# Performance work log

Measured on AMD Instinct MI355X. Metric: run time of the kernel, lower is better.

Reference implementation:

```python
import jax, jax.numpy as jnp
import numpy as np

NUM_GRAPHS = 8
NEG_SLOPE = 0.2


def add_self_loops(edge_index, n):
    loops = jnp.arange(n, dtype=edge_index.dtype)
    src = jnp.concatenate([edge_index[0], loops])
    dst = jnp.concatenate([edge_index[1], loops])
    return src, dst


def gat_conv(x, src, dst, W, att_src, att_dst, bias, concat):
    # x: [N, F_in]; W: [F_in, H*C]; att_src/att_dst: [H, C]; bias: [H*C] or [C]
    n = x.shape[0]
    H, C = att_src.shape
    xl = (x @ W).reshape(n, H, C)                     # [N, H, C]
    a_src = jnp.einsum('nhc,hc->nh', xl, att_src)     # [N, H]
    a_dst = jnp.einsum('nhc,hc->nh', xl, att_dst)     # [N, H]
    e = jax.nn.leaky_relu(a_src[src] + a_dst[dst], NEG_SLOPE)  # [E, H]
    # segment softmax over edges grouped by destination node
    m = jax.ops.segment_max(e, dst, num_segments=n)   # [N, H]
    e = jnp.exp(e - m[dst])
    denom = jax.ops.segment_sum(e, dst, num_segments=n)
    alpha = e / (denom[dst] + 1e-16)                  # [E, H]
    msg = xl[src] * alpha[:, :, None]                 # [E, H, C]
    out = jax.ops.segment_sum(msg, dst, num_segments=n)  # [N, H, C]
    out = out.reshape(n, H * C) if concat else out.mean(axis=1)
    return out + bias


def global_mean_pool(x, batch, num_graphs):
    s = jax.ops.segment_sum(x, batch, num_segments=num_graphs)
    cnt = jax.ops.segment_sum(jnp.ones((x.shape[0],), x.dtype), batch, num_segments=num_graphs)
    return s / jnp.maximum(cnt, 1.0)[:, None]


def setup_inputs() -> dict:
    key = jax.random.key(0)
    ks = jax.random.split(key, 12)
    N, E, F_in, Ch, H, F_out = 50000, 800000, 128, 64, 4, 128
    x = jax.random.normal(ks[0], (N, F_in), dtype=jnp.float32)
    edge_index = jax.random.randint(ks[1], (2, E), 0, N, dtype=jnp.int64)
    batch = jnp.sort(jax.random.randint(ks[2], (N,), 0, NUM_GRAPHS, dtype=jnp.int64))
    s = 0.1
    W1 = jax.random.normal(ks[3], (F_in, H * Ch), dtype=jnp.float32) * s
    att_src1 = jax.random.normal(ks[4], (H, Ch), dtype=jnp.float32) * s
    att_dst1 = jax.random.normal(ks[5], (H, Ch), dtype=jnp.float32) * s
    bias1 = jnp.zeros((H * Ch,), dtype=jnp.float32)
    W2 = jax.random.normal(ks[6], (H * Ch, F_out), dtype=jnp.float32) * s
    att_src2 = jax.random.normal(ks[7], (1, F_out), dtype=jnp.float32) * s
    att_dst2 = jax.random.normal(ks[8], (1, F_out), dtype=jnp.float32) * s
    bias2 = jnp.zeros((F_out,), dtype=jnp.float32)
    return {"x": x, "edge_index": edge_index, "batch": batch,
            "W1": W1, "att_src1": att_src1, "att_dst1": att_dst1, "bias1": bias1,
            "W2": W2, "att_src2": att_src2, "att_dst2": att_dst2, "bias2": bias2}


def reference(x, edge_index, batch, W1, att_src1, att_dst1, bias1, W2, att_src2, att_dst2, bias2):
    n = x.shape[0]
    src, dst = add_self_loops(edge_index, n)
    h = gat_conv(x, src, dst, W1, att_src1, att_dst1, bias1, concat=True)
    h = jax.nn.relu(h)
    h = gat_conv(h, src, dst, W2, att_src2, att_dst2, bias2, concat=False)
    return global_mean_pool(h, batch, NUM_GRAPHS)
```

## Files before the change

kernel.cpp:

```cpp
#include <hip/hip_runtime.h>
#include <cstdint>
#include <cstddef>

#define NEG_SLOPE 0.2f
#define LOG2E 1.44269504088896f

typedef __attribute__((ext_vector_type(8))) short bf16x8;
typedef __attribute__((ext_vector_type(4))) float f32x4;
typedef __attribute__((ext_vector_type(2))) float f32x2;

__device__ __forceinline__ ushort f2b(float f) {
  unsigned u = __float_as_uint(f);
  return (ushort)((u + 0x7FFFu + ((u >> 16) & 1)) >> 16);
}
__device__ __forceinline__ float fexp2(float x) {
#if __has_builtin(__builtin_amdgcn_exp2f)
  return __builtin_amdgcn_exp2f(x);
#else
  return __exp2f(x);
#endif
}
__device__ __forceinline__ int lbound(const int* __restrict__ a, int n, int key) {
  int lo = 0, hi = n;
  while (lo < hi) { int m = (lo + hi) >> 1; if (a[m] < key) lo = m + 1; else hi = m; }
  return lo;
}

__global__ __launch_bounds__(256) void pack_w_both(const float* __restrict__ W1,
                                                   ushort* __restrict__ Bp1,
                                                   const float* __restrict__ W2,
                                                   ushort* __restrict__ Bp2) {
  int i = blockIdx.x * 256 + threadIdx.x;
  if (i >= 128 * 256) return;
  {
    int k = i >> 8, n = i & 255;
    Bp1[(((size_t)(k >> 3) * 256 + n) << 3) + (k & 7)] = f2b(W1[i]);
  }
  {
    int k = i >> 7, n = i & 127;
    Bp2[(((size_t)(k >> 3) * 128 + n) << 3) + (k & 7)] = f2b(W2[i]);
  }
}

template<int N, int K, int C, int H, bool AF32>
__global__ __launch_bounds__(256) void gemm_attn(const void* __restrict__ A_,
                                                 const ushort* __restrict__ Bp,
                                                 const float* __restrict__ att_src,
                                                 const float* __restrict__ att_dst,
                                                 unsigned char* __restrict__ C8,
                                                 float* __restrict__ a_src,
                                                 float* __restrict__ a_dst, int M) {
  const int wave = threadIdx.x >> 6;
  const int lane = threadIdx.x & 63;
  const int strips = M / 16;
  const int strip = blockIdx.x * 4 + wave;
  if (strip >= strips) return;
  const int r = lane & 15, kg = lane >> 4;
  const int row = strip * 16 + r;

  bf16x8 a[K / 32];
  if constexpr (AF32) {
    const float* Af = (const float*)A_;
    #pragma unroll
    for (int k0 = 0; k0 < K / 32; ++k0) {
      float4 f0 = *(const float4*)(Af + (size_t)row * K + k0 * 32 + kg * 8);
      float4 f1 = *(const float4*)(Af + (size_t)row * K + k0 * 32 + kg * 8 + 4);
      bf16x8 t;
      t[0] = (short)f2b(f0.x); t[1] = (short)f2b(f0.y);
      t[2] = (short)f2b(f0.z); t[3] = (short)f2b(f0.w);
      t[4] = (short)f2b(f1.x); t[5] = (short)f2b(f1.y);
      t[6] = (short)f2b(f1.z); t[7] = (short)f2b(f1.w);
      a[k0] = t;
    }
  } else {
    const ushort* Ab = (const ushort*)A_;
    #pragma unroll
    for (int k0 = 0; k0 < K / 32; ++k0)
      a[k0] = *(const bf16x8*)(Ab + (size_t)row * K + k0 * 32 + kg * 8);
  }

  float as_part[4] = {}, ad_part[4] = {};
  #pragma unroll 2
  for (int n0 = 0; n0 < N / 16; ++n0) {
    f32x4 acc = {0.f, 0.f, 0.f, 0.f};
    #pragma unroll
    for (int k0 = 0; k0 < K / 32; ++k0) {
      bf16x8 b = *(const bf16x8*)(Bp + ((size_t)(k0 * 4 + kg) * N + n0 * 16 + r) * 8);
      acc = __builtin_amdgcn_mfma_f32_16x16x32_bf16(a[k0], b, acc, 0, 0, 0);
    }
    float asv = att_src[n0 * 16 + r] * LOG2E;
    float adv = att_dst[n0 * 16 + r] * LOG2E;
    #pragma unroll
    for (int i = 0; i < 4; ++i) {
      as_part[i] = fmaf(acc[i], asv, as_part[i]);
      ad_part[i] = fmaf(acc[i], adv, ad_part[i]);
    }
    #pragma unroll
    for (int i = 0; i < 4; ++i) {
      int pk = __builtin_amdgcn_cvt_pk_fp8_f32(acc[i], acc[i], 0, false);
      C8[((size_t)strip * 16 + kg * 4 + i) * N + n0 * 16 + r] = (unsigned char)(pk & 0xFF);
    }
    if (((n0 + 1) * 16) % C == 0) {
      int h = (n0 * 16) / C;
      #pragma unroll
      for (int i = 0; i < 4; ++i) {
        float ts = as_part[i], td = ad_part[i];
        #pragma unroll
        for (int off = 1; off < 16; off <<= 1) {
          ts += __shfl_xor(ts, off);
          td += __shfl_xor(td, off);
        }
        if (r == i) {
          a_src[(size_t)(strip * 16 + kg * 4 + i) * H + h] = ts;
          a_dst[(size_t)(strip * 16 + kg * 4 + i) * H + h] = td;
        }
        as_part[i] = 0.f;
        ad_part[i] = 0.f;
      }
    }
  }
}

__global__ __launch_bounds__(256) void rank_k(const int* __restrict__ edst,
                                              int* __restrict__ hist,
                                              int* __restrict__ rank, int E) {
  int e = blockIdx.x * 256 + threadIdx.x;
  if (e >= E) return;
  rank[e] = atomicAdd(hist + edst[e], 1);
}

__global__ __launch_bounds__(256) void scan1_k(const int* __restrict__ hist,
                                               int* __restrict__ excl,
                                               int* __restrict__ chunksum, int n) {
  __shared__ int sums[256];
  int base = blockIdx.x * 1024 + threadIdx.x * 4;
  int4 v = {0, 0, 0, 0};
  if (base + 3 < n) v = *(const int4*)(hist + base);
  else {
    if (base < n)     v.x = hist[base];
    if (base + 1 < n) v.y = hist[base + 1];
    if (base + 2 < n) v.z = hist[base + 2];
    if (base + 3 < n) v.w = hist[base + 3];
  }
  int s = v.x + v.y + v.z + v.w;
  sums[threadIdx.x] = s;
  __syncthreads();
  for (int off = 1; off < 256; off <<= 1) {
    int t = (threadIdx.x >= (unsigned)off) ? sums[threadIdx.x - off] : 0;
    __syncthreads();
    sums[threadIdx.x] += t;
    __syncthreads();
  }
  if (threadIdx.x == 255) chunksum[blockIdx.x] = sums[255];
  int e0 = sums[threadIdx.x] - s;
  int e1 = e0 + v.x, e2 = e1 + v.y, e3 = e2 + v.z;
  if (base + 3 < n) {
    int4 o = {e0, e1, e2, e3};
    *(int4*)(excl + base) = o;
  } else {
    if (base < n)     excl[base] = e0;
    if (base + 1 < n) excl[base + 1] = e1;
    if (base + 2 < n) excl[base + 2] = e2;
    if (base + 3 < n) excl[base + 3] = e3;
  }
}

__global__ void scan2_k(const int* __restrict__ chunksum,
                        int* __restrict__ chunkoff, int nchunks) {
  if (threadIdx.x == 0) {
    int run = 0;
    for (int c = 0; c < nchunks; ++c) { chunkoff[c] = run; run += chunksum[c]; }
  }
}

__global__ __launch_bounds__(256) void addoff_k(int* __restrict__ rowptr,
                                                const int* __restrict__ chunkoff,
                                                int n, int total) {
  int i = blockIdx.x * 256 + threadIdx.x;
  if (i == 0) rowptr[n] = total;
  if (i >= n) return;
  rowptr[i] += chunkoff[i >> 10];
}

__global__ __launch_bounds__(256) void fill_k(const int* __restrict__ esrc,
                                              const int* __restrict__ edst,
                                              const int* __restrict__ rowptr,
                                              const int* __restrict__ rank,
                                              int* __restrict__ csr_src,
                                              int E, int Epad) {
  int e = blockIdx.x * 256 + threadIdx.x;
  if (e < E) csr_src[rowptr[edst[e]] + rank[e]] = esrc[e];
  else if (e < Epad) csr_src[e] = 0;
}

template<int H, int C>
__global__ __launch_bounds__(256) void agg1_k(const int* __restrict__ rowptr,
                                              const int* __restrict__ csr,
                                              const float* __restrict__ a_src,
                                              const float* __restrict__ a_dst,
                                              const unsigned char* __restrict__ xl,
                                              const float* __restrict__ bias,
                                              ushort* __restrict__ out, int n) {
  constexpr int F = H * C;
  const int wid0 = (blockIdx.x * 256 + threadIdx.x) >> 6;
  if (wid0 >= n) return;
  const int wid = __builtin_amdgcn_readfirstlane(wid0);
  const int lane = threadIdx.x & 63;
  const int h = lane >> 4;
  const uint lofs = (uint)lane * 4;
  const int j4 = lane & 3;
  const int je = lane >> 2;
  const int beg = rowptr[wid];
  const int end = rowptr[wid + 1];

  const float adh_s = a_dst[(uint)wid * 4 + j4];
  float vs_s = a_src[(uint)wid * 4 + j4] + adh_s;
  vs_s = fmaxf(vs_s, NEG_SLOPE * vs_s);

  float den = 1.f;
  float acc[4];
  {
    uint xs = *(const uint*)(xl + ((uint)wid * F + lofs));
    f32x2 lo = __builtin_amdgcn_cvt_pk_f32_fp8(xs, false);
    f32x2 hi = __builtin_amdgcn_cvt_pk_f32_fp8(xs, true);
    acc[0] = lo[0]; acc[1] = lo[1]; acc[2] = hi[0]; acc[3] = hi[1];
  }

  for (int j = beg; j < end; j += 16) {
    int sl = csr[j + je];
    float t = a_src[(uint)sl * 4 + j4] + adh_s;
    t = fmaxf(t, NEG_SLOPE * t);
    t = (j + je < end) ? t - vs_s : -1e30f;
    float pl = fexp2(t);
    uint xv[16];
    #pragma unroll
    for (int u = 0; u < 16; ++u) {
      int su = csr[j + u];
      xv[u] = *(const uint*)(xl + ((uint)su * F + lofs));
    }
    #pragma unroll
    for (int u = 0; u < 16; ++u) {
      float pu = __shfl(pl, u * 4 + h);
      den += pu;
      f32x2 lo = __builtin_amdgcn_cvt_pk_f32_fp8(xv[u], false);
      f32x2 hi = __builtin_amdgcn_cvt_pk_f32_fp8(xv[u], true);
      acc[0] = fmaf(pu, lo[0], acc[0]);
      acc[1] = fmaf(pu, lo[1], acc[1]);
      acc[2] = fmaf(pu, hi[0], acc[2]);
      acc[3] = fmaf(pu, hi[1], acc[3]);
    }
  }

  float inv = 1.f / (den + 1e-16f);
  float o[4];
  #pragma unroll
  for (int i = 0; i < 4; ++i)
    o[i] = fmaxf(fmaf(acc[i], inv, bias[lane * 4 + i]), 0.f);
  ushort4 ov = {f2b(o[0]), f2b(o[1]), f2b(o[2]), f2b(o[3])};
  *(ushort4*)(out + (size_t)wid * F + lane * 4) = ov;
}

__global__ __launch_bounds__(256) void agg2_k(const int* __restrict__ rowptr,
                                              const int* __restrict__ csr,
                                              const float* __restrict__ a_src,
                                              const float* __restrict__ a_dst,
                                              const unsigned char* __restrict__ xl,
                                              float* __restrict__ out2,
                                              int n, int Emax) {
  const int pair = (blockIdx.x * 256 + threadIdx.x) >> 6;
  const int lane = threadIdx.x & 63;
  const int l32 = lane & 31;
  const int half = lane >> 5;
  int wid = pair * 2 + half;
  const bool act = wid < n;
  if (!act) wid = n - 1;
  const uint lofs = (uint)l32 * 4;
  const int beg = rowptr[wid];
  const int deg = rowptr[wid + 1] - beg;
  const int mdeg = max(deg, __shfl_xor(deg, 32));
  const float adh = a_dst[wid];

  float vs = a_src[wid] + adh;
  vs = fmaxf(vs, NEG_SLOPE * vs);
  float den = 1.f;
  float acc[4];
  {
    uint xs = *(const uint*)(xl + ((uint)wid * 128 + lofs));
    f32x2 lo = __builtin_amdgcn_cvt_pk_f32_fp8(xs, false);
    f32x2 hi = __builtin_amdgcn_cvt_pk_f32_fp8(xs, true);
    acc[0] = lo[0]; acc[1] = lo[1]; acc[2] = hi[0]; acc[3] = hi[1];
  }

  for (int j = 0; j < mdeg; j += 32) {
    int sl = csr[min(beg + j + l32, Emax)];
    float t = a_src[sl] + adh;
    t = fmaxf(t, NEG_SLOPE * t);
    t = (j + l32 < deg) ? t - vs : -1e30f;
    float pl = fexp2(t);
    #pragma unroll
    for (int g = 0; g < 2; ++g) {
      int su[16];
      uint xv[16];
      #pragma unroll
      for (int u = 0; u < 16; ++u) {
        su[u] = __shfl(sl, half * 32 + g * 16 + u);
        xv[u] = *(const uint*)(xl + ((uint)su[u] * 128 + lofs));
      }
      #pragma unroll
      for (int u = 0; u < 16; ++u) {
        float pu = __shfl(pl, half * 32 + g * 16 + u);
        den += pu;
        f32x2 lo = __builtin_amdgcn_cvt_pk_f32_fp8(xv[u], false);
        f32x2 hi = __builtin_amdgcn_cvt_pk_f32_fp8(xv[u], true);
        acc[0] = fmaf(pu, lo[0], acc[0]);
        acc[1] = fmaf(pu, lo[1], acc[1]);
        acc[2] = fmaf(pu, hi[0], acc[2]);
        acc[3] = fmaf(pu, hi[1], acc[3]);
      }
    }
  }

  if (act) {
    float inv = 1.f / (den + 1e-16f);
    float4 ov = {acc[0] * inv, acc[1] * inv, acc[2] * inv, acc[3] * inv};
    *(float4*)(out2 + (size_t)wid * 128 + l32 * 4) = ov;
  }
}

__global__ __launch_bounds__(256) void pool2_k(const float* __restrict__ out2,
                                               const int* __restrict__ batch,
                                               float* __restrict__ pp, int n) {
  const int g = blockIdx.y;
  const int b = blockIdx.x;
  const int lo = lbound(batch, n, g);
  const int hi = lbound(batch, n, g + 1);
  const int cnt = hi - lo;
  const int span = (cnt + 31) >> 5;
  const int s0 = lo + b * span;
  const int s1 = min(s0 + span, hi);
  const int qid = threadIdx.x & 31;
  const int phase = threadIdx.x >> 5;

  float4 a = {0.f, 0.f, 0.f, 0.f};
  for (int node = s0 + phase; node < s1; node += 8) {
    float4 v = *(const float4*)(out2 + (size_t)node * 128 + qid * 4);
    a.x += v.x; a.y += v.y; a.z += v.z; a.w += v.w;
  }
  __shared__ float red[8][128];
  *(float4*)&red[phase][qid * 4] = a;
  __syncthreads();
  if (threadIdx.x < 128) {
    float s = 0.f;
    #pragma unroll
    for (int ph = 0; ph < 8; ++ph) s += red[ph][threadIdx.x];
    pp[((size_t)g * 32 + b) * 128 + threadIdx.x] = s;
  }
}

__global__ __launch_bounds__(256) void finalize_k(const float* __restrict__ pp,
                                                  const int* __restrict__ batch,
                                                  const float* __restrict__ bias2,
                                                  float* __restrict__ out, int n) {
  int t = blockIdx.x * 256 + threadIdx.x;
  if (t >= 8 * 128) return;
  int g = t >> 7, c = t & 127;
  float s = 0.f;
  #pragma unroll
  for (int b = 0; b < 32; ++b) s += pp[((size_t)g * 32 + b) * 128 + c];
  int lo = lbound(batch, n, g);
  int hi = lbound(batch, n, g + 1);
  float cnt = (float)(hi - lo);
  out[t] = s / fmaxf(cnt, 1.f) + bias2[c];
}

extern "C" void kernel_launch(void* const* d_in, const int* in_sizes, int n_in,
                              void* d_out, int out_size, void* d_ws, size_t ws_size,
                              hipStream_t stream) {
  const float* x        = (const float*)d_in[0];
  const int*   ei       = (const int*)d_in[1];
  const int*   batch    = (const int*)d_in[2];
  const float* W1       = (const float*)d_in[3];
  const float* att_src1 = (const float*)d_in[4];
  const float* att_dst1 = (const float*)d_in[5];
  const float* bias1    = (const float*)d_in[6];
  const float* W2       = (const float*)d_in[7];
  const float* att_src2 = (const float*)d_in[8];
  const float* att_dst2 = (const float*)d_in[9];
  const float* bias2    = (const float*)d_in[10];
  float* out = (float*)d_out;

  const int E  = in_sizes[1] / 2;
  const int NN = in_sizes[2];
  const int* esrc = ei;
  const int* edst = ei + E;
  const int PAD = 64;

  char* w = (char*)d_ws;
  size_t woff = 0;
  auto walloc = [&](size_t bytes) -> char* {
    char* r = w + woff;
    woff += (bytes + 255) & ~(size_t)255;
    return r;
  };
  unsigned char* xl1 = (unsigned char*)walloc((size_t)NN * 256);
  ushort* h1     = (ushort*)walloc((size_t)NN * 256 * 2);
  unsigned char* xl2 = (unsigned char*)walloc((size_t)NN * 128);
  float*  a_src1 = (float*)walloc((size_t)NN * 4 * 4);
  float*  a_dst1 = (float*)walloc((size_t)NN * 4 * 4);
  float*  a_src2 = (float*)walloc((size_t)NN * 4);
  float*  a_dst2 = (float*)walloc((size_t)NN * 4);
  int*    rowptr = (int*)walloc((size_t)(NN + 1) * 4);
  int*    hist   = (int*)walloc((size_t)NN * 4);
  int*    rank   = (int*)walloc((size_t)E * 4);
  int*    csrsrc = (int*)walloc((size_t)(E + PAD) * 4);
  ushort* Bp1    = (ushort*)walloc(128 * 256 * 2);
  ushort* Bp2    = (ushort*)walloc(256 * 128 * 2);
  int*    chunks = (int*)walloc(256 * 4);
  int*    chunko = (int*)walloc(256 * 4);
  float*  pp     = (float*)walloc(8 * 32 * 128 * 4);
  float*  out2   = (float*)h1;

  dim3 blk(256);
  const int nbE  = (E + 255) / 256;
  const int nbEp = (E + PAD + 255) / 256;
  const int nbN4 = (NN + 3) / 4;
  const int nbP  = ((NN + 1) / 2 + 3) / 4;
  const int nchunks = (NN + 1023) / 1024;
  const int gblocks = (NN / 16 + 3) / 4;

  hipMemsetAsync(hist, 0, (size_t)NN * 4, stream);
  rank_k<<<nbE, blk, 0, stream>>>(edst, hist, rank, E);
  scan1_k<<<nchunks, blk, 0, stream>>>(hist, rowptr, chunks, NN);
  scan2_k<<<1, 64, 0, stream>>>(chunks, chunko, nchunks);
  addoff_k<<<(NN + 255) / 256, blk, 0, stream>>>(rowptr, chunko, NN, E);
  fill_k<<<nbEp, blk, 0, stream>>>(esrc, edst, rowptr, rank, csrsrc, E, E + PAD);

  pack_w_both<<<(128 * 256 + 255) / 256, blk, 0, stream>>>(W1, Bp1, W2, Bp2);

  gemm_attn<256, 128, 64, 4, true><<<gblocks, blk, 0, stream>>>(
      x, Bp1, att_src1, att_dst1, xl1, a_src1, a_dst1, NN);
  agg1_k<4, 64><<<nbN4, blk, 0, stream>>>(
      rowptr, csrsrc, a_src1, a_dst1, xl1, bias1, h1, NN);

  gemm_attn<128, 256, 128, 1, false><<<gblocks, blk, 0, stream>>>(
      h1, Bp2, att_src2, att_dst2, xl2, a_src2, a_dst2, NN);
  agg2_k<<<nbP, blk, 0, stream>>>(
      rowptr, csrsrc, a_src2, a_dst2, xl2, out2, NN, E + PAD - 1);

  {
    dim3 grid2(32, 8);
    pool2_k<<<grid2, blk, 0, stream>>>(out2, batch, pp, NN);
  }
  finalize_k<<<4, blk, 0, stream>>>(pp, batch, bias2, out, NN);
}
```

Before: 188.9 us.

## Fuse setup kernels, rank into GEMM launch, single-block scan, pooling into agg2

Merges the weight packing, histogram memset and pool-buffer zeroing into one setup kernel. The edge-rank atomics now run as extra blocks of the first GEMM launch, and the three-kernel scan becomes a single 1024-thread block. The second aggregation reduces its outputs per graph in shared memory and atomically adds them into 64 replicated partial buffers, which removes the out2 write/read and the separate pool kernel. This cuts launch count and memory traffic, at the cost of a serial single-block scan and of atomic contention in the pool.

```diff
diff --git a/kernel.cpp b/kernel.cpp
--- a/kernel.cpp
+++ b/kernel.cpp
@@ -4,6 +4,7 @@
 
 #define NEG_SLOPE 0.2f
 #define LOG2E 1.44269504088896f
+#define NREP 64
 
 typedef __attribute__((ext_vector_type(8))) short bf16x8;
 typedef __attribute__((ext_vector_type(4))) float f32x4;
@@ -26,34 +27,41 @@
   return lo;
 }
 
-__global__ __launch_bounds__(256) void pack_w_both(const float* __restrict__ W1,
-                                                   ushort* __restrict__ Bp1,
-                                                   const float* __restrict__ W2,
-                                                   ushort* __restrict__ Bp2) {
+__global__ __launch_bounds__(256) void setup_k(const float* __restrict__ W1,
+                                               ushort* __restrict__ Bp1,
+                                               const float* __restrict__ W2,
+                                               ushort* __restrict__ Bp2,
+                                               int* __restrict__ hist,
+                                               float* __restrict__ pp, int n) {
   int i = blockIdx.x * 256 + threadIdx.x;
-  if (i >= 128 * 256) return;
   {
-    int k = i >> 8, n = i & 255;
-    Bp1[(((size_t)(k >> 3) * 256 + n) << 3) + (k & 7)] = f2b(W1[i]);
+    int k = i >> 8, c = i & 255;
+    Bp1[(((size_t)(k >> 3) * 256 + c) << 3) + (k & 7)] = f2b(W1[i]);
   }
   {
-    int k = i >> 7, n = i & 127;
-    Bp2[(((size_t)(k >> 3) * 128 + n) << 3) + (k & 7)] = f2b(W2[i]);
-  }
+    int k = i >> 7, c = i & 127;
+    Bp2[(((size_t)(k >> 3) * 128 + c) << 3) + (k & 7)] = f2b(W2[i]);
+  }
+  if (i < n) hist[i] = 0;
+  int i2 = i + 32768;
+  if (i2 < n) hist[i2] = 0;
+  pp[i] = 0.f;
+  pp[i + 32768] = 0.f;
 }
 
 template<int N, int K, int C, int H, bool AF32>
-__global__ __launch_bounds__(256) void gemm_attn(const void* __restrict__ A_,
-                                                 const ushort* __restrict__ Bp,
-                                                 const float* __restrict__ att_src,
-                                                 const float* __restrict__ att_dst,
-                                                 unsigned char* __restrict__ C8,
-                                                 float* __restrict__ a_src,
-                                                 float* __restrict__ a_dst, int M) {
+__device__ __forceinline__ void gemm_attn_body(const void* __restrict__ A_,
+                                               const ushort* __restrict__ Bp,
+                                               const float* __restrict__ att_src,
+                                               const float* __restrict__ att_dst,
+                                               unsigned char* __restrict__ C8,
+                                               float* __restrict__ a_src,
+                                               float* __restrict__ a_dst,
+                                               int M, int bid) {
   const int wave = threadIdx.x >> 6;
   const int lane = threadIdx.x & 63;
   const int strips = M / 16;
-  const int strip = blockIdx.x * 4 + wave;
+  const int strip = bid * 4 + wave;
   if (strip >= strips) return;
   const int r = lane & 15, kg = lane >> 4;
   const int row = strip * 16 + r;
@@ -121,65 +129,64 @@
   }
 }
 
-__global__ __launch_bounds__(256) void rank_k(const int* __restrict__ edst,
-                                              int* __restrict__ hist,
-                                              int* __restrict__ rank, int E) {
-  int e = blockIdx.x * 256 + threadIdx.x;
-  if (e >= E) return;
-  rank[e] = atomicAdd(hist + edst[e], 1);
-}
-
-__global__ __launch_bounds__(256) void scan1_k(const int* __restrict__ hist,
-                                               int* __restrict__ excl,
-                                               int* __restrict__ chunksum, int n) {
-  __shared__ int sums[256];
-  int base = blockIdx.x * 1024 + threadIdx.x * 4;
-  int4 v = {0, 0, 0, 0};
-  if (base + 3 < n) v = *(const int4*)(hist + base);
-  else {
-    if (base < n)     v.x = hist[base];
-    if (base + 1 < n) v.y = hist[base + 1];
-    if (base + 2 < n) v.z = hist[base + 2];
-    if (base + 3 < n) v.w = hist[base + 3];
-  }
-  int s = v.x + v.y + v.z + v.w;
-  sums[threadIdx.x] = s;
+template<int N, int K, int C, int H, bool AF32>
+__global__ __launch_bounds__(256) void gemm_rank_k(const void* __restrict__ A_,
+                                                   const ushort* __restrict__ Bp,
+                                                   const float* __restrict__ att_src,
+                                                   const float* __restrict__ att_dst,
+                                                   unsigned char* __restrict__ C8,
+                                                   float* __restrict__ a_src,
+                                                   float* __restrict__ a_dst, int M,
+                                                   const int* __restrict__ edst,
+                                                   int* __restrict__ hist,
+                                                   int* __restrict__ rank,
+                                                   int E, int GB) {
+  if ((int)blockIdx.x < GB) {
+    gemm_attn_body<N, K, C, H, AF32>(A_, Bp, att_src, att_dst, C8, a_src, a_dst,
+                                     M, blockIdx.x);
+  } else {
+    int base = ((blockIdx.x - GB) * 256 + threadIdx.x) * 8;
+    #pragma unroll
+    for (int u = 0; u < 8; ++u) {
+      int e = base + u;
+      if (e < E) rank[e] = atomicAdd(hist + edst[e], 1);
+    }
+  }
+}
+
+template<int N, int K, int C, int H, bool AF32>
+__global__ __launch_bounds__(256) void gemm_attn_k(const void* __restrict__ A_,
+                                                   const ushort* __restrict__ Bp,
+                                                   const float* __restrict__ att_src,
+                                                   const float* __restrict__ att_dst,
+                                                   unsigned char* __restrict__ C8,
+                                                   float* __restrict__ a_src,
+                                                   float* __restrict__ a_dst, int M) {
+  gemm_attn_body<N, K, C, H, AF32>(A_, Bp, att_src, att_dst, C8, a_src, a_dst,
+                                   M, blockIdx.x);
+}
+
+__global__ __launch_bounds__(1024) void scan_fused_k(const int* __restrict__ hist,
+                                                     int* __restrict__ rowptr,
+                                                     int n, int total) {
+  __shared__ int sums[1024];
+  const int t = threadIdx.x;
+  const int per = (n + 1023) / 1024;
+  const int s0 = min(t * per, n);
+  const int s1 = min(s0 + per, n);
+  int s = 0;
+  for (int i = s0; i < s1; ++i) s += hist[i];
+  sums[t] = s;
   __syncthreads();
-  for (int off = 1; off < 256; off <<= 1) {
-    int t = (threadIdx.x >= (unsigned)off) ? sums[threadIdx.x - off] : 0;
+  for (int off = 1; off < 1024; off <<= 1) {
+    int v = (t >= off) ? sums[t - off] : 0;
     __syncthreads();
-    sums[threadIdx.x] += t;
+    sums[t] += v;
     __syncthreads();
   }
-  if (threadIdx.x == 255) chunksum[blockIdx.x] = sums[255];
-  int e0 = sums[threadIdx.x] - s;
-  int e1 = e0 + v.x, e2 = e1 + v.y, e3 = e2 + v.z;
-  if (base + 3 < n) {
-    int4 o = {e0, e1, e2, e3};
-    *(int4*)(excl + base) = o;
-  } else {
-    if (base < n)     excl[base] = e0;
-    if (base + 1 < n) excl[base + 1] = e1;
-    if (base + 2 < n) excl[base + 2] = e2;
-    if (base + 3 < n) excl[base + 3] = e3;
-  }
-}
-
-__global__ void scan2_k(const int* __restrict__ chunksum,
-                        int* __restrict__ chunkoff, int nchunks) {
-  if (threadIdx.x == 0) {
-    int run = 0;
-    for (int c = 0; c < nchunks; ++c) { chunkoff[c] = run; run += chunksum[c]; }
-  }
-}
-
-__global__ __launch_bounds__(256) void addoff_k(int* __restrict__ rowptr,
-                                                const int* __restrict__ chunkoff,
-                                                int n, int total) {
-  int i = blockIdx.x * 256 + threadIdx.x;
-  if (i == 0) rowptr[n] = total;
-  if (i >= n) return;
-  rowptr[i] += chunkoff[i >> 10];
+  int run = sums[t] - s;
+  for (int i = s0; i < s1; ++i) { rowptr[i] = run; run += hist[i]; }
+  if (t == 0) rowptr[n] = total;
 }
 
 __global__ __launch_bounds__(256) void fill_k(const int* __restrict__ esrc,
@@ -260,13 +267,14 @@
   *(ushort4*)(out + (size_t)wid * F + lane * 4) = ov;
 }
 
-__global__ __launch_bounds__(256) void agg2_k(const int* __restrict__ rowptr,
-                                              const int* __restrict__ csr,
-                                              const float* __restrict__ a_src,
-                                              const float* __restrict__ a_dst,
-                                              const unsigned char* __restrict__ xl,
-                                              float* __restrict__ out2,
-                                              int n, int Emax) {
+__global__ __launch_bounds__(256) void agg2pool_k(const int* __restrict__ rowptr,
+                                                  const int* __restrict__ csr,
+                                                  const float* __restrict__ a_src,
+                                                  const float* __restrict__ a_dst,
+                                                  const unsigned char* __restrict__ xl,
+                                                  const int* __restrict__ batch,
+                                                  float* __restrict__ pp,
+                                                  int n, int Emax) {
   const int pair = (blockIdx.x * 256 + threadIdx.x) >> 6;
   const int lane = threadIdx.x & 63;
   const int l32 = lane & 31;
@@ -320,40 +328,30 @@
     }
   }
 
-  if (act) {
-    float inv = 1.f / (den + 1e-16f);
-    float4 ov = {acc[0] * inv, acc[1] * inv, acc[2] * inv, acc[3] * inv};
-    *(float4*)(out2 + (size_t)wid * 128 + l32 * 4) = ov;
-  }
-}
-
-__global__ __launch_bounds__(256) void pool2_k(const float* __restrict__ out2,
-                                               const int* __restrict__ batch,
-                                               float* __restrict__ pp, int n) {
-  const int g = blockIdx.y;
-  const int b = blockIdx.x;
-  const int lo = lbound(batch, n, g);
-  const int hi = lbound(batch, n, g + 1);
-  const int cnt = hi - lo;
-  const int span = (cnt + 31) >> 5;
-  const int s0 = lo + b * span;
-  const int s1 = min(s0 + span, hi);
-  const int qid = threadIdx.x & 31;
-  const int phase = threadIdx.x >> 5;
-
-  float4 a = {0.f, 0.f, 0.f, 0.f};
-  for (int node = s0 + phase; node < s1; node += 8) {
-    float4 v = *(const float4*)(out2 + (size_t)node * 128 + qid * 4);
-    a.x += v.x; a.y += v.y; a.z += v.z; a.w += v.w;
-  }
   __shared__ float red[8][128];
-  *(float4*)&red[phase][qid * 4] = a;
+  __shared__ int gids[8];
+  const int rrow = (threadIdx.x >> 6) * 2 + half;
+  float inv = act ? 1.f / (den + 1e-16f) : 0.f;
+  float4 ov = {acc[0] * inv, acc[1] * inv, acc[2] * inv, acc[3] * inv};
+  *(float4*)&red[rrow][l32 * 4] = ov;
+  if (l32 == 0) gids[rrow] = act ? batch[wid] : -1;
   __syncthreads();
   if (threadIdx.x < 128) {
-    float s = 0.f;
-    #pragma unroll
-    for (int ph = 0; ph < 8; ++ph) s += red[ph][threadIdx.x];
-    pp[((size_t)g * 32 + b) * 128 + threadIdx.x] = s;
+    const int ch = threadIdx.x;
+    float* base = pp + (size_t)(blockIdx.x & (NREP - 1)) * 8 * 128;
+    float sum = 0.f;
+    int cur = gids[0];
+    #pragma unroll
+    for (int r = 0; r < 8; ++r) {
+      int g = gids[r];
+      if (g != cur) {
+        if (cur >= 0) unsafeAtomicAdd(base + cur * 128 + ch, sum);
+        sum = 0.f;
+        cur = g;
+      }
+      if (g >= 0) sum += red[r][ch];
+    }
+    if (cur >= 0) unsafeAtomicAdd(base + cur * 128 + ch, sum);
   }
 }
 
@@ -365,8 +363,8 @@
   if (t >= 8 * 128) return;
   int g = t >> 7, c = t & 127;
   float s = 0.f;
-  #pragma unroll
-  for (int b = 0; b < 32; ++b) s += pp[((size_t)g * 32 + b) * 128 + c];
+  #pragma unroll 8
+  for (int rep = 0; rep < NREP; ++rep) s += pp[rep * 8 * 128 + t];
   int lo = lbound(batch, n, g);
   int hi = lbound(batch, n, g + 1);
   float cnt = (float)(hi - lo);
@@ -415,41 +413,33 @@
   int*    csrsrc = (int*)walloc((size_t)(E + PAD) * 4);
   ushort* Bp1    = (ushort*)walloc(128 * 256 * 2);
   ushort* Bp2    = (ushort*)walloc(256 * 128 * 2);
-  int*    chunks = (int*)walloc(256 * 4);
-  int*    chunko = (int*)walloc(256 * 4);
-  float*  pp     = (float*)walloc(8 * 32 * 128 * 4);
-  float*  out2   = (float*)h1;
+  float*  pp     = (float*)walloc((size_t)NREP * 8 * 128 * 4);
 
   dim3 blk(256);
-  const int nbE  = (E + 255) / 256;
   const int nbEp = (E + PAD + 255) / 256;
   const int nbN4 = (NN + 3) / 4;
   const int nbP  = ((NN + 1) / 2 + 3) / 4;
-  const int nchunks = (NN + 1023) / 1024;
   const int gblocks = (NN / 16 + 3) / 4;
-
-  hipMemsetAsync(hist, 0, (size_t)NN * 4, stream);
-  rank_k<<<nbE, blk, 0, stream>>>(edst, hist, rank, E);
-  scan1_k<<<nchunks, blk, 0, stream>>>(hist, rowptr, chunks, NN);
-  scan2_k<<<1, 64, 0, stream>>>(chunks, chunko, nchunks);
-  addoff_k<<<(NN + 255) / 256, blk, 0, stream>>>(rowptr, chunko, NN, E);
+  const int rankBlocks = (E + 2047) / 2048;
+
+  setup_k<<<128, blk, 0, stream>>>(W1, Bp1, W2, Bp2, hist, pp, NN);
+
+  gemm_rank_k<256, 128, 64, 4, true><<<gblocks + rankBlocks, blk, 0, stream>>>(
+      x, Bp1, att_src1, att_dst1, xl1, a_src1, a_dst1, NN,
+      edst, hist, rank, E, gblocks);
+
+  scan_fused_k<<<1, 1024, 0, stream>>>(hist, rowptr, NN, E);
+
   fill_k<<<nbEp, blk, 0, stream>>>(esrc, edst, rowptr, rank, csrsrc, E, E + PAD);
 
-  pack_w_both<<<(128 * 256 + 255) / 256, blk, 0, stream>>>(W1, Bp1, W2, Bp2);
-
-  gemm_attn<256, 128, 64, 4, true><<<gblocks, blk, 0, stream>>>(
-      x, Bp1, att_src1, att_dst1, xl1, a_src1, a_dst1, NN);
   agg1_k<4, 64><<<nbN4, blk, 0, stream>>>(
       rowptr, csrsrc, a_src1, a_dst1, xl1, bias1, h1, NN);
 
-  gemm_attn<128, 256, 128, 1, false><<<gblocks, blk, 0, stream>>>(
+  gemm_attn_k<128, 256, 128, 1, false><<<gblocks, blk, 0, stream>>>(
       h1, Bp2, att_src2, att_dst2, xl2, a_src2, a_dst2, NN);
-  agg2_k<<<nbP, blk, 0, stream>>>(
-      rowptr, csrsrc, a_src2, a_dst2, xl2, out2, NN, E + PAD - 1);
-
-  {
-    dim3 grid2(32, 8);
-    pool2_k<<<grid2, blk, 0, stream>>>(out2, batch, pp, NN);
-  }
+
+  agg2pool_k<<<nbP, blk, 0, stream>>>(
+      rowptr, csrsrc, a_src2, a_dst2, xl2, batch, pp, NN, E + PAD - 1);
+
   finalize_k<<<4, blk, 0, stream>>>(pp, batch, bias2, out, NN);
 }
```

Result: slower. 227.8 us (+20.6%).
